# Kernel tuning notes

Measured on AMD Instinct MI355X. Metric: run time of the kernel, lower is better.

Reference implementation:

```python
import jax, jax.numpy as jnp
import numpy as np

WAY = 5
SHOT = 5
NEIGHBOR_K = 3


def setup_inputs() -> dict:
    key = jax.random.key(0)
    k1, k2 = jax.random.split(key)
    x1 = jax.random.normal(k1, (75, 640, 21, 21), dtype=jnp.float32)   # queries
    x2 = jax.random.normal(k2, (25, 640, 21, 21), dtype=jnp.float32)   # support (way*shot)
    return {"x1": x1, "x2": x2}


def reference(x1, x2):
    Q, C, H, W = x1.shape
    S = x2.shape[0]  # way * shot
    HW = H * W

    # queries: [Q, C, HW] -> [Q, HW, C], L2-normalize each local descriptor
    q = jnp.transpose(x1.reshape(Q, C, HW), (0, 2, 1))
    q = q / jnp.linalg.norm(q, axis=2, keepdims=True)

    # support: [S, HW, C], normalize, regroup per class: [way, shot*HW, C]
    s = jnp.transpose(x2.reshape(S, C, HW), (0, 2, 1))
    s = s / jnp.linalg.norm(s, axis=2, keepdims=True)
    s = s.reshape(WAY, SHOT * HW, C)

    # cosine similarity of every query descriptor vs every class descriptor
    # [Q, way, HW, shot*HW]
    sim = jnp.einsum('qmc,wnc->qwmn', q, s)

    # top-k neighbors per query descriptor along class-descriptor axis, then sum
    topk_vals, _ = jax.lax.top_k(sim, NEIGHBOR_K)   # [Q, way, HW, k]
    img2class_sim = jnp.sum(topk_vals, axis=(2, 3))  # [Q, way]
    return img2class_sim
```

## Files before the change

### kernel.cpp

```cpp
#include <hip/hip_runtime.h>

typedef unsigned char u8;
typedef int i32x4 __attribute__((ext_vector_type(4)));
typedef int i32x16 __attribute__((ext_vector_type(16)));

#define C_DIM 640
#define HW_DIM 441
#define QN 75
#define SN 25
#define WAYS 5
#define MROWS 33075
#define MCH   128
#define MBLK  259
#define MPAD  33152
#define NWAY  2205
#define NPAD  2304
#define BN    256
#define NT    9
#define INV_Q2 (1.0f / 16129.0f)
#define NEGINF (-2147483647 - 1)

__device__ __forceinline__ void glds16(const void* g, void* l) {
  __builtin_amdgcn_global_load_lds(
      (__attribute__((address_space(1))) unsigned int*)g,
      (__attribute__((address_space(3))) unsigned int*)l, 16, 0, 0);
}

__global__ void zero_pad(u8* __restrict__ A8, u8* __restrict__ S8,
                         float* __restrict__ out) {
  int i = blockIdx.x * 256 + threadIdx.x;
  if (i < 49280) {
    A8[(size_t)MROWS * C_DIM + i] = 0;
    return;
  }
  i -= 49280;
  if (i < 316800) {
    const int w = i / 63360;
    const int r = i % 63360;
    S8[((size_t)w * NPAD + NWAY) * C_DIM + r] = 0;
    return;
  }
  i -= 316800;
  if (i < QN * WAYS) out[i] = 0.f;
}

__global__ __launch_bounds__(256)
void prep_norm_transpose(const float* __restrict__ src, u8* __restrict__ dst,
                         int support) {
  const int bid = blockIdx.x;
  const int img = bid / 7;
  const int mt = bid % 7;
  const int m0 = mt * 64;
  const int t = threadIdx.x;
  const int mloc = t & 63;
  const int cpart = t >> 6;
  const int m = m0 + mloc;
  const int m_eff = (m < HW_DIM) ? m : (HW_DIM - 1);
  const float* base = src + (size_t)img * (C_DIM * HW_DIM);

  float ss = 0.f;
  const int c0 = cpart * 160;
  for (int c = c0; c < c0 + 160; ++c) {
    float v = base[(size_t)c * HW_DIM + m_eff];
    ss += v * v;
  }
  __shared__ float red[256];
  __shared__ float inv[64];
  red[t] = ss;
  __syncthreads();
  if (t < 64) {
    float s4 = red[t] + red[t + 64] + red[t + 128] + red[t + 192];
    inv[t] = rsqrtf(s4) * 127.0f;
  }
  __syncthreads();

  size_t drow0;
  if (support) {
    const int w = img / 5, shot = img % 5;
    drow0 = (size_t)w * NPAD + (size_t)shot * HW_DIM;
  } else {
    drow0 = (size_t)img * HW_DIM;
  }

  __shared__ __align__(16) u8 T[64][80];
  const float iv = inv[mloc];
  const int mw = t >> 2;
  const int cg = t & 3;
  const int m_out = m0 + mw;

  for (int ct = 0; ct < 10; ++ct) {
    int q[16];
#pragma unroll
    for (int ci = 0; ci < 16; ++ci) {
      const int c = ct * 64 + cpart * 16 + ci;
      q[ci] = __float2int_rn(base[(size_t)c * HW_DIM + m_eff] * iv);
    }
    __syncthreads();
    uint4 w;
    w.x = (q[0] & 255) | ((q[1] & 255) << 8) | ((q[2] & 255) << 16) | ((q[3] & 255) << 24);
    w.y = (q[4] & 255) | ((q[5] & 255) << 8) | ((q[6] & 255) << 16) | ((q[7] & 255) << 24);
    w.z = (q[8] & 255) | ((q[9] & 255) << 8) | ((q[10] & 255) << 16) | ((q[11] & 255) << 24);
    w.w = (q[12] & 255) | ((q[13] & 255) << 8) | ((q[14] & 255) << 16) | ((q[15] & 255) << 24);
    *(uint4*)&T[mloc][cpart * 16] = w;
    __syncthreads();
    if (m_out < HW_DIM) {
      const uint4 v = *(const uint4*)&T[mw][cg * 16];
      *(uint4*)(dst + (drow0 + m_out) * C_DIM + ct * 64 + cg * 16) = v;
    }
  }
}

__global__ __launch_bounds__(512, 2)
void simtopk(const u8* __restrict__ A8, const u8* __restrict__ S8,
             float* __restrict__ out) {
  __shared__ __align__(16) u8 As[MCH * C_DIM];
  __shared__ __align__(16) u8 Bs[2][BN * 128];
  __shared__ float qsum[2];

  const int bid = blockIdx.x;
  const int way = bid / MBLK;
  const int mc = bid % MBLK;
  const int R0 = mc * MCH;
  const int tid = threadIdx.x;
  const int lane = tid & 63;
  const int wv = tid >> 6;
  const int wmB = (wv >> 2) * 64;
  const int wnB = (wv & 3) * 64;
  const int r5 = lane & 31;
  const int h = lane >> 5;

  if (tid < 2) qsum[tid] = 0.f;

  const u8* Sway = S8 + (size_t)way * NPAD * C_DIM;
  const u8* Ab = A8 + (size_t)R0 * C_DIM;

#pragma unroll
  for (int i = 0; i < 10; ++i) {
    const int id = wv * 10 + i;
    const int oct = id / 5, i2 = id % 5;
    const int lin = i2 * 64 + lane;
    const int row = lin / 40;
    const int quad = lin % 40;
    const int sq = (quad & ~7) | ((quad & 7) ^ (row & 7));
    glds16(Ab + (unsigned)(oct * 5120 + row * 640 + sq * 16),
           As + oct * 5120 + i2 * 1024);
  }

  const unsigned brow =
      (unsigned)((lane >> 3) * 640 + (((lane & 7) ^ (lane >> 3)) * 16));
#pragma unroll
  for (int j = 0; j < 4; ++j) {
    const int st = wv * 4 + j;
    glds16(Sway + (unsigned)st * (8 * 640) + brow, Bs[0] + st * 1024);
  }

  int aAddr[2][4], bAddr[2][4];
#pragma unroll
  for (int s = 0; s < 4; ++s) {
    const int pq = ((2 * s + h) ^ (r5 & 7)) * 16;
#pragma unroll
    for (int mi = 0; mi < 2; ++mi)
      aAddr[mi][s] = (wmB + mi * 32 + r5) * 640 + pq;
#pragma unroll
    for (int ni = 0; ni < 2; ++ni)
      bAddr[ni][s] = (wnB + ni * 32 + r5) * 128 + pq;
  }

  i32x16 acc[2][2];
#pragma unroll
  for (int mi = 0; mi < 2; ++mi)
#pragma unroll
    for (int ni = 0; ni < 2; ++ni)
#pragma unroll
      for (int g = 0; g < 16; ++g) acc[mi][ni][g] = 0;

  int t0[32], t1[32], t2[32];
#pragma unroll
  for (int r = 0; r < 32; ++r) { t0[r] = NEGINF; t1[r] = NEGINF; t2[r] = NEGINF; }

  int p = 0;
  for (int nt = 0; nt < NT; ++nt) {
#pragma unroll
    for (int kt = 0; kt < 5; ++kt) {
      __syncthreads();

      if (!(nt == NT - 1 && kt == 4)) {
        const int nt1 = (kt == 4) ? nt + 1 : nt;
        const int kt1 = (kt == 4) ? 0 : kt + 1;
        const unsigned off =
            (unsigned)nt1 * (BN * C_DIM) + (unsigned)(kt1 * 128);
#pragma unroll
        for (int j = 0; j < 4; ++j) {
          const int st = wv * 4 + j;
          glds16(Sway + (unsigned)st * (8 * 640) + brow + off,
                 Bs[p ^ 1] + st * 1024);
        }
      }

      const u8* Bp = Bs[p];
      const int ka = kt * 128;
#pragma unroll
      for (int s = 0; s < 4; ++s) {
        const i32x4 a0 = *(const i32x4*)(As + aAddr[0][s] + ka);
        const i32x4 a1 = *(const i32x4*)(As + aAddr[1][s] + ka);
        const i32x4 b0 = *(const i32x4*)(Bp + bAddr[0][s]);
        const i32x4 b1 = *(const i32x4*)(Bp + bAddr[1][s]);
        acc[0][0] = __builtin_amdgcn_mfma_i32_32x32x32_i8(a0, b0, acc[0][0], 0, 0, 0);
        acc[1][0] = __builtin_amdgcn_mfma_i32_32x32x32_i8(a1, b0, acc[1][0], 0, 0, 0);
        acc[0][1] = __builtin_amdgcn_mfma_i32_32x32x32_i8(a0, b1, acc[0][1], 0, 0, 0);
        acc[1][1] = __builtin_amdgcn_mfma_i32_32x32x32_i8(a1, b1, acc[1][1], 0, 0, 0);
      }
      p ^= 1;
    }

    const bool lastT = (nt == NT - 1);
#pragma unroll
    for (int ni = 0; ni < 2; ++ni) {
      const int ncol = nt * BN + wnB + ni * 32 + r5;
      const bool bad = lastT && (ncol >= NWAY);
#pragma unroll
      for (int mi = 0; mi < 2; ++mi)
#pragma unroll
        for (int g = 0; g < 16; ++g) {
          int v = acc[mi][ni][g];
          if (bad) v = NEGINF;
          const int r = mi * 16 + g;
          t2[r] = max(t2[r], min(v, t1[r]));
          t1[r] = max(t1[r], min(v, t0[r]));
          t0[r] = max(t0[r], v);
          acc[mi][ni][g] = 0;
        }
    }
  }

#pragma unroll
  for (int d = 1; d <= 2; d <<= 1) {
#pragma unroll
    for (int r = 0; r < 32; ++r) {
      const int o0 = __shfl_xor(t0[r], d);
      const int o1 = __shfl_xor(t1[r], d);
      const int o2 = __shfl_xor(t2[r], d);
      t2[r] = max(t2[r], min(o0, t1[r]));
      t1[r] = max(t1[r], min(o0, t0[r]));
      t0[r] = max(t0[r], o0);
      t2[r] = max(t2[r], min(o1, t1[r]));
      t1[r] = max(t1[r], min(o1, t0[r]));
      t0[r] = max(t0[r], o1);
      t2[r] = max(t2[r], min(o2, t1[r]));
      t1[r] = max(t1[r], min(o2, t0[r]));
      t0[r] = max(t0[r], o2);
    }
  }

  __syncthreads();
  int* part = (int*)&Bs[0][0];
  if ((r5 & 3) == 0) {
    const int nq = wv & 3;
    const int grp = nq * 8 + (r5 >> 2);
#pragma unroll
    for (int r = 0; r < 32; ++r) {
      const int mi = r >> 4, g = r & 15;
      const int row_local = wmB + mi * 32 + (g & 3) + 8 * (g >> 2) + 4 * h;
      i32x4 v;
      v[0] = t0[r]; v[1] = t1[r]; v[2] = t2[r]; v[3] = NEGINF;
      *(i32x4*)&part[(row_local * 32 + grp) * 4] = v;
    }
  }
  __syncthreads();
  if (tid < MCH) {
    const int grow = R0 + tid;
    if (grow < MROWS) {
      int a0 = NEGINF, a1 = NEGINF, a2 = NEGINF;
#pragma unroll 4
      for (int j = 0; j < 32; ++j) {
        const int jj = (j + tid) & 31;
        const i32x4 v = *(const i32x4*)&part[(tid * 32 + jj) * 4];
        a2 = max(a2, min(v[0], a1)); a1 = max(a1, min(v[0], a0)); a0 = max(a0, v[0]);
        a2 = max(a2, min(v[1], a1)); a1 = max(a1, min(v[1], a0)); a0 = max(a0, v[1]);
        a2 = max(a2, min(v[2], a1)); a1 = max(a1, min(v[2], a0)); a0 = max(a0, v[2]);
      }
      const float rs = (float)(a0 + a1 + a2) * INV_Q2;
      const int qq = grow / HW_DIM;
      atomicAdd(&qsum[qq - (R0 / HW_DIM)], rs);
    }
  }
  __syncthreads();
  if (tid < 2) {
    const int qq = R0 / HW_DIM + tid;
    if (qq < QN) atomicAdd(out + qq * WAYS + way, qsum[tid]);
  }
}

extern "C" void kernel_launch(void* const* d_in, const int* in_sizes, int n_in,
                              void* d_out, int out_size, void* d_ws, size_t ws_size,
                              hipStream_t stream) {
  const float* x1 = (const float*)d_in[0];
  const float* x2 = (const float*)d_in[1];
  float* out = (float*)d_out;
  u8* A8 = (u8*)d_ws;
  u8* S8 = (u8*)d_ws + (size_t)MPAD * C_DIM;

  hipLaunchKernelGGL(zero_pad, dim3(1432), dim3(256), 0, stream, A8, S8, out);
  hipLaunchKernelGGL(prep_norm_transpose, dim3(QN * 7), dim3(256), 0, stream,
                     x1, A8, 0);
  hipLaunchKernelGGL(prep_norm_transpose, dim3(SN * 7), dim3(256), 0, stream,
                     x2, S8, 1);
  hipLaunchKernelGGL(simtopk, dim3(WAYS * MBLK), dim3(512), 0, stream,
                     A8, S8, out);
}
```

Baseline: 560.3 us.

## Keep A tile in registers, shrink block to 64 rows with 4 waves

The simtopk kernel no longer stages the query tile in LDS. Each wave loads its 32 query rows across the full K dimension straight into 20 i32x4 registers, and the block shrinks to 64 rows and 256 threads, doubling the grid. This removes the 80KB A tile from shared memory and the LDS reads for A, which should allow more blocks per CU. The costs are more register pressure, doubled streaming of the support matrix from L2 (each B tile now serves only 64 rows), and a reworked partial top-k reduction layout.

```diff
diff --git a/kernel.cpp b/kernel.cpp
--- a/kernel.cpp
+++ b/kernel.cpp
@@ -10,9 +10,9 @@
 #define SN 25
 #define WAYS 5
 #define MROWS 33075
-#define MCH   128
-#define MBLK  259
-#define MPAD  33152
+#define MCH   64
+#define MBLK  517
+#define MPAD  33088
 #define NWAY  2205
 #define NPAD  2304
 #define BN    256
@@ -29,11 +29,11 @@
 __global__ void zero_pad(u8* __restrict__ A8, u8* __restrict__ S8,
                          float* __restrict__ out) {
   int i = blockIdx.x * 256 + threadIdx.x;
-  if (i < 49280) {
+  if (i < 8320) {
     A8[(size_t)MROWS * C_DIM + i] = 0;
     return;
   }
-  i -= 49280;
+  i -= 8320;
   if (i < 316800) {
     const int w = i / 63360;
     const int r = i % 63360;
@@ -110,10 +110,9 @@
   }
 }
 
-__global__ __launch_bounds__(512, 2)
+__global__ __launch_bounds__(256, 2)
 void simtopk(const u8* __restrict__ A8, const u8* __restrict__ S8,
              float* __restrict__ out) {
-  __shared__ __align__(16) u8 As[MCH * C_DIM];
   __shared__ __align__(16) u8 Bs[2][BN * 128];
   __shared__ float qsum[2];
 
@@ -124,59 +123,49 @@
   const int tid = threadIdx.x;
   const int lane = tid & 63;
   const int wv = tid >> 6;
-  const int wmB = (wv >> 2) * 64;
-  const int wnB = (wv & 3) * 64;
+  const int wm = (wv >> 1) * 32;
+  const int nh = wv & 1;
+  const int wnB = nh * 128;
   const int r5 = lane & 31;
   const int h = lane >> 5;
 
   if (tid < 2) qsum[tid] = 0.f;
 
   const u8* Sway = S8 + (size_t)way * NPAD * C_DIM;
-  const u8* Ab = A8 + (size_t)R0 * C_DIM;
-
-#pragma unroll
-  for (int i = 0; i < 10; ++i) {
-    const int id = wv * 10 + i;
-    const int oct = id / 5, i2 = id % 5;
-    const int lin = i2 * 64 + lane;
-    const int row = lin / 40;
-    const int quad = lin % 40;
-    const int sq = (quad & ~7) | ((quad & 7) ^ (row & 7));
-    glds16(Ab + (unsigned)(oct * 5120 + row * 640 + sq * 16),
-           As + oct * 5120 + i2 * 1024);
+
+  i32x4 a[20];
+  {
+    const u8* Arow = A8 + (size_t)(R0 + wm + r5) * C_DIM + h * 16;
+#pragma unroll
+    for (int ks = 0; ks < 20; ++ks)
+      a[ks] = *(const i32x4*)(Arow + ks * 32);
   }
 
   const unsigned brow =
       (unsigned)((lane >> 3) * 640 + (((lane & 7) ^ (lane >> 3)) * 16));
 #pragma unroll
-  for (int j = 0; j < 4; ++j) {
-    const int st = wv * 4 + j;
+  for (int j = 0; j < 8; ++j) {
+    const int st = wv * 8 + j;
     glds16(Sway + (unsigned)st * (8 * 640) + brow, Bs[0] + st * 1024);
   }
 
-  int aAddr[2][4], bAddr[2][4];
-#pragma unroll
-  for (int s = 0; s < 4; ++s) {
-    const int pq = ((2 * s + h) ^ (r5 & 7)) * 16;
-#pragma unroll
-    for (int mi = 0; mi < 2; ++mi)
-      aAddr[mi][s] = (wmB + mi * 32 + r5) * 640 + pq;
-#pragma unroll
-    for (int ni = 0; ni < 2; ++ni)
-      bAddr[ni][s] = (wnB + ni * 32 + r5) * 128 + pq;
-  }
-
-  i32x16 acc[2][2];
-#pragma unroll
-  for (int mi = 0; mi < 2; ++mi)
-#pragma unroll
-    for (int ni = 0; ni < 2; ++ni)
-#pragma unroll
-      for (int g = 0; g < 16; ++g) acc[mi][ni][g] = 0;
-
-  int t0[32], t1[32], t2[32];
-#pragma unroll
-  for (int r = 0; r < 32; ++r) { t0[r] = NEGINF; t1[r] = NEGINF; t2[r] = NEGINF; }
+  int bBase[4], pqs[4];
+#pragma unroll
+  for (int ni = 0; ni < 4; ++ni)
+    bBase[ni] = (wnB + ni * 32 + r5) * 128;
+#pragma unroll
+  for (int s = 0; s < 4; ++s)
+    pqs[s] = ((2 * s + h) ^ (r5 & 7)) * 16;
+
+  i32x16 acc[4];
+#pragma unroll
+  for (int ni = 0; ni < 4; ++ni)
+#pragma unroll
+    for (int g = 0; g < 16; ++g) acc[ni][g] = 0;
+
+  int t0[16], t1[16], t2[16];
+#pragma unroll
+  for (int r = 0; r < 16; ++r) { t0[r] = NEGINF; t1[r] = NEGINF; t2[r] = NEGINF; }
 
   int p = 0;
   for (int nt = 0; nt < NT; ++nt) {
@@ -190,53 +179,50 @@
         const unsigned off =
             (unsigned)nt1 * (BN * C_DIM) + (unsigned)(kt1 * 128);
 #pragma unroll
-        for (int j = 0; j < 4; ++j) {
-          const int st = wv * 4 + j;
+        for (int j = 0; j < 8; ++j) {
+          const int st = wv * 8 + j;
           glds16(Sway + (unsigned)st * (8 * 640) + brow + off,
                  Bs[p ^ 1] + st * 1024);
         }
       }
 
       const u8* Bp = Bs[p];
-      const int ka = kt * 128;
 #pragma unroll
       for (int s = 0; s < 4; ++s) {
-        const i32x4 a0 = *(const i32x4*)(As + aAddr[0][s] + ka);
-        const i32x4 a1 = *(const i32x4*)(As + aAddr[1][s] + ka);
-        const i32x4 b0 = *(const i32x4*)(Bp + bAddr[0][s]);
-        const i32x4 b1 = *(const i32x4*)(Bp + bAddr[1][s]);
-        acc[0][0] = __builtin_amdgcn_mfma_i32_32x32x32_i8(a0, b0, acc[0][0], 0, 0, 0);
-        acc[1][0] = __builtin_amdgcn_mfma_i32_32x32x32_i8(a1, b0, acc[1][0], 0, 0, 0);
-        acc[0][1] = __builtin_amdgcn_mfma_i32_32x32x32_i8(a0, b1, acc[0][1], 0, 0, 0);
-        acc[1][1] = __builtin_amdgcn_mfma_i32_32x32x32_i8(a1, b1, acc[1][1], 0, 0, 0);
+        const i32x4 av = a[kt * 4 + s];
+        i32x4 b0 = *(const i32x4*)(Bp + bBase[0] + pqs[s]);
+        i32x4 b1 = *(const i32x4*)(Bp + bBase[1] + pqs[s]);
+        i32x4 b2 = *(const i32x4*)(Bp + bBase[2] + pqs[s]);
+        i32x4 b3 = *(const i32x4*)(Bp + bBase[3] + pqs[s]);
+        acc[0] = __builtin_amdgcn_mfma_i32_32x32x32_i8(av, b0, acc[0], 0, 0, 0);
+        acc[1] = __builtin_amdgcn_mfma_i32_32x32x32_i8(av, b1, acc[1], 0, 0, 0);
+        acc[2] = __builtin_amdgcn_mfma_i32_32x32x32_i8(av, b2, acc[2], 0, 0, 0);
+        acc[3] = __builtin_amdgcn_mfma_i32_32x32x32_i8(av, b3, acc[3], 0, 0, 0);
       }
       p ^= 1;
     }
 
     const bool lastT = (nt == NT - 1);
 #pragma unroll
-    for (int ni = 0; ni < 2; ++ni) {
+    for (int ni = 0; ni < 4; ++ni) {
       const int ncol = nt * BN + wnB + ni * 32 + r5;
       const bool bad = lastT && (ncol >= NWAY);
 #pragma unroll
-      for (int mi = 0; mi < 2; ++mi)
-#pragma unroll
-        for (int g = 0; g < 16; ++g) {
-          int v = acc[mi][ni][g];
-          if (bad) v = NEGINF;
-          const int r = mi * 16 + g;
-          t2[r] = max(t2[r], min(v, t1[r]));
-          t1[r] = max(t1[r], min(v, t0[r]));
-          t0[r] = max(t0[r], v);
-          acc[mi][ni][g] = 0;
-        }
+      for (int g = 0; g < 16; ++g) {
+        int v = acc[ni][g];
+        if (bad) v = NEGINF;
+        t2[g] = max(t2[g], min(v, t1[g]));
+        t1[g] = max(t1[g], min(v, t0[g]));
+        t0[g] = max(t0[g], v);
+        acc[ni][g] = 0;
+      }
     }
   }
 
 #pragma unroll
   for (int d = 1; d <= 2; d <<= 1) {
 #pragma unroll
-    for (int r = 0; r < 32; ++r) {
+    for (int r = 0; r < 16; ++r) {
       const int o0 = __shfl_xor(t0[r], d);
       const int o1 = __shfl_xor(t1[r], d);
       const int o2 = __shfl_xor(t2[r], d);
@@ -255,15 +241,13 @@
   __syncthreads();
   int* part = (int*)&Bs[0][0];
   if ((r5 & 3) == 0) {
-    const int nq = wv & 3;
-    const int grp = nq * 8 + (r5 >> 2);
-#pragma unroll
-    for (int r = 0; r < 32; ++r) {
-      const int mi = r >> 4, g = r & 15;
-      const int row_local = wmB + mi * 32 + (g & 3) + 8 * (g >> 2) + 4 * h;
+    const int grp = nh * 8 + (r5 >> 2);
+#pragma unroll
+    for (int r = 0; r < 16; ++r) {
+      const int row_local = wm + (r & 3) + 8 * (r >> 2) + 4 * h;
       i32x4 v;
       v[0] = t0[r]; v[1] = t1[r]; v[2] = t2[r]; v[3] = NEGINF;
-      *(i32x4*)&part[(row_local * 32 + grp) * 4] = v;
+      *(i32x4*)&part[(grp * MCH + row_local) * 4] = v;
     }
   }
   __syncthreads();
@@ -272,9 +256,8 @@
     if (grow < MROWS) {
       int a0 = NEGINF, a1 = NEGINF, a2 = NEGINF;
 #pragma unroll 4
-      for (int j = 0; j < 32; ++j) {
-        const int jj = (j + tid) & 31;
-        const i32x4 v = *(const i32x4*)&part[(tid * 32 + jj) * 4];
+      for (int g = 0; g < 16; ++g) {
+        const i32x4 v = *(const i32x4*)&part[(g * MCH + tid) * 4];
         a2 = max(a2, min(v[0], a1)); a1 = max(a1, min(v[0], a0)); a0 = max(a0, v[0]);
         a2 = max(a2, min(v[1], a1)); a1 = max(a1, min(v[1], a0)); a0 = max(a0, v[1]);
         a2 = max(a2, min(v[2], a1)); a1 = max(a1, min(v[2], a0)); a0 = max(a0, v[2]);
@@ -300,11 +283,11 @@
   u8* A8 = (u8*)d_ws;
   u8* S8 = (u8*)d_ws + (size_t)MPAD * C_DIM;
 
-  hipLaunchKernelGGL(zero_pad, dim3(1432), dim3(256), 0, stream, A8, S8, out);
+  hipLaunchKernelGGL(zero_pad, dim3(1272), dim3(256), 0, stream, A8, S8, out);
   hipLaunchKernelGGL(prep_norm_transpose, dim3(QN * 7), dim3(256), 0, stream,
                      x1, A8, 0);
   hipLaunchKernelGGL(prep_norm_transpose, dim3(SN * 7), dim3(256), 0, stream,
                      x2, S8, 1);
-  hipLaunchKernelGGL(simtopk, dim3(WAYS * MBLK), dim3(512), 0, stream,
+  hipLaunchKernelGGL(simtopk, dim3(WAYS * MBLK), dim3(256), 0, stream,
                      A8, S8, out);
 }
```

Result: faster. 538.2 us (-4.0%).
